# Performance work log

Measured on AMD Instinct MI355X. Metric: run time of the kernel, lower is better.

Reference implementation:

```python
import jax, jax.numpy as jnp
import numpy as np

ADIM = 128
VDIM = 64

def setup_inputs() -> dict:
    key = jax.random.key(0)
    ks = jax.random.split(key, 12)
    B, N, E = 4, 10000, 320000
    pos_0 = jax.random.normal(ks[0], (B, N, 3), dtype=jnp.float32)
    pos_1 = jax.random.normal(ks[1], (B, N, 3), dtype=jnp.float32)
    src = jax.random.randint(ks[2], (E,), 0, N, dtype=jnp.int64)
    dst = jax.random.randint(ks[3], (E,), 0, N, dtype=jnp.int64)
    # parameters (torch default inits approximated; randn for VecLinear as in source)
    Wv = jax.random.normal(ks[4], (VDIM, 6), dtype=jnp.float32)
    def lin(k, fan_in, fan_out):
        kw, kb = jax.random.split(k)
        bound = 1.0 / np.sqrt(fan_in)
        W = jax.random.uniform(kw, (fan_out, fan_in), minval=-bound, maxval=bound, dtype=jnp.float32)
        b = jax.random.uniform(kb, (fan_out,), minval=-bound, maxval=bound, dtype=jnp.float32)
        return W, b
    W1, b1 = lin(ks[5], 6, ADIM)
    W2, b2 = lin(ks[6], ADIM, ADIM)
    W3, b3 = lin(ks[7], ADIM, ADIM)
    return {"pos_0": pos_0, "pos_1": pos_1, "src": src, "dst": dst,
            "Wv": Wv, "W1": W1, "b1": b1, "W2": W2, "b2": b2, "W3": W3, "b3": b3}

def _leaky(x):
    return jnp.where(x >= 0, x, 0.2 * x)

def reference(pos_0, pos_1, src, dst, Wv, W1, b1, W2, b2, W3, b3):
    # gather endpoint positions: (B, E, 3)
    p0s = jnp.take(pos_0, src, axis=1)
    p0d = jnp.take(pos_0, dst, axis=1)
    p1s = jnp.take(pos_1, src, axis=1)
    p1d = jnp.take(pos_1, dst, axis=1)
    # 6 relative vectors: (B, E, 6, 3)
    vecs = jnp.stack([p0d - p0s, p1d - p1s, p1s - p0s, p1d - p0d, p1s - p0d, p1d - p0s], axis=2)
    norms = jnp.sqrt(jnp.sum(vecs * vecs, axis=-1))  # (B, E, 6)
    h = _leaky(jnp.einsum('bei,oi->beo', norms, W1) + b1)
    h = _leaky(jnp.einsum('bei,oi->beo', h, W2) + b2)
    a_out = jnp.einsum('bei,oi->beo', h, W3) + b3  # (B, E, ADIM)
    v_out = jnp.einsum('oi,beik->beok', Wv, vecs) / 3  # (B, E, VDIM, 3)
    return (a_out, v_out)
```

## Files before the change

kernel.cpp:

```cpp
#include <hip/hip_runtime.h>

#define NB 4
#define NN 10000
#define NE 320000
#define EPB 128
#define NBLK ((NB * NE) / EPB)

typedef unsigned int uint;
typedef unsigned short ushort;
typedef __attribute__((ext_vector_type(8))) short short8;
typedef __attribute__((ext_vector_type(4))) float f32x4;

#define WS_W1T 0
#define WS_W2T 8192
#define WS_W3T 40960
#define WS_WVT 73728

static __device__ __forceinline__ ushort f2bf(float f) {
    uint u = __float_as_uint(f);
    u += 0x7fffu + ((u >> 16) & 1u);
    return (ushort)(u >> 16);
}
static __device__ __forceinline__ uint pack2(float a, float b) {
    return (uint)f2bf(a) | ((uint)f2bf(b) << 16);
}
static __device__ __forceinline__ uint cvtpk(float a, float b) {
    uint r;
    asm("v_cvt_pk_bf16_f32 %0, %1, %2" : "=v"(r) : "v"(a), "v"(b));
    return r;
}
static __device__ __forceinline__ short8 u4s8(uint4 v) {
    union { uint4 u; short8 s; } x; x.u = v; return x.s;
}
static __device__ __forceinline__ f32x4 MF(uint4 a, uint4 b, f32x4 c) {
    return __builtin_amdgcn_mfma_f32_16x16x32_bf16(u4s8(a), u4s8(b), c, 0, 0, 0);
}

__global__ void prep_kernel(const float* __restrict__ W1, const float* __restrict__ W2,
                            const float* __restrict__ W3, const float* __restrict__ Wv,
                            unsigned char* __restrict__ ws) {
    int tid = blockIdx.x * blockDim.x + threadIdx.x;
    if (tid < 4096) {
        const float* W = (tid < 2048) ? W2 : W3;
        uint4* dst = (uint4*)(ws + ((tid < 2048) ? WS_W2T : WS_W3T));
        int f = tid & 2047;
        int lane = f & 63, kt = (f >> 6) & 3, mt = (f >> 8) & 7;
        int la = lane >> 4, lm = lane & 15;
        int n = mt * 16 + lm;
        uint w[4];
        #pragma unroll
        for (int jw = 0; jw < 4; ++jw) {
            int j0 = jw * 2, j1 = j0 + 1;
            int k0 = kt * 32 + (j0 >> 2) * 16 + la * 4 + (j0 & 3);
            int k1 = kt * 32 + (j1 >> 2) * 16 + la * 4 + (j1 & 3);
            w[jw] = pack2(W[n * 128 + k0], W[n * 128 + k1]);
        }
        dst[f] = make_uint4(w[0], w[1], w[2], w[3]);
    } else if (tid < 4608) {
        int f = tid - 4096;
        int lane = f & 63, mt = f >> 6;
        int la = lane >> 4, lm = lane & 15;
        int n = mt * 16 + lm;
        uint w[4];
        #pragma unroll
        for (int jw = 0; jw < 4; ++jw) {
            int j0 = jw * 2, j1 = j0 + 1;
            int k0 = (j0 >> 2) * 16 + la * 4 + (j0 & 3);
            int k1 = (j1 >> 2) * 16 + la * 4 + (j1 & 3);
            float f0 = (k0 < 6) ? W1[n * 6 + k0] : 0.f;
            float f1 = (k1 < 6) ? W1[n * 6 + k1] : 0.f;
            w[jw] = pack2(f0, f1);
        }
        ((uint4*)(ws + WS_W1T))[f] = make_uint4(w[0], w[1], w[2], w[3]);
    } else if (tid < 5376) {
        int f = tid - 4608;
        int lane = f & 63, mt = f >> 6;
        int la = lane >> 4, lm = lane & 15;
        int row = mt * 16 + lm;
        int o = row / 3, c = row - o * 3;
        uint w[4];
        #pragma unroll
        for (int jw = 0; jw < 4; ++jw) {
            float vv[2];
            #pragma unroll
            for (int dc = 0; dc < 2; ++dc) {
                int j = jw * 2 + dc;
                int k = (j >> 2) * 16 + la * 4 + (j & 3);
                int i = k / 3, cc = k - i * 3;
                vv[dc] = (k < 18 && cc == c) ? Wv[o * 6 + i] * (1.f / 3.f) : 0.f;
            }
            w[jw] = pack2(vv[0], vv[1]);
        }
        ((uint4*)(ws + WS_WVT))[f] = make_uint4(w[0], w[1], w[2], w[3]);
    }
}

__global__ __launch_bounds__(256, 3)
void edge_kernel(const float* __restrict__ pos0, const float* __restrict__ pos1,
                 const int* __restrict__ src, const int* __restrict__ dstI,
                 const float* __restrict__ b1, const float* __restrict__ b2,
                 const float* __restrict__ b3,
                 const unsigned char* __restrict__ ws, float* __restrict__ out) {
    __shared__ float s_pts[128][13];
    __shared__ float s_vecs[128][20];
    __shared__ float s_norms[6][128];

    const int tid = threadIdx.x;
    const int lane = tid & 63;
    const int w = tid >> 6;
    const int lm = lane & 15;
    const int la = lane >> 4;
    const int ew0 = w * 32;

    const int bid = blockIdx.x;
    const int b = bid / (NE / EPB);
    const int e0 = (bid % (NE / EPB)) * EPB;
    const size_t eg0 = (size_t)b * NE + e0;

    const uint4* W1T = (const uint4*)(ws + WS_W1T);
    const uint4* W2T = (const uint4*)(ws + WS_W2T);
    const uint4* W3T = (const uint4*)(ws + WS_W3T);
    const uint4* WVT = (const uint4*)(ws + WS_WVT);

    {
        const int el = ew0 + (lane & 31);
        const int side = lane >> 5;
        const int e = e0 + el;
        const int node = side ? dstI[e] : src[e];
        const size_t pb = ((size_t)b * NN + node) * 3;
        float a0 = pos0[pb], a1 = pos0[pb + 1], a2 = pos0[pb + 2];
        float c0 = pos1[pb], c1 = pos1[pb + 1], c2 = pos1[pb + 2];
        s_pts[el][side * 3 + 0] = a0;
        s_pts[el][side * 3 + 1] = a1;
        s_pts[el][side * 3 + 2] = a2;
        s_pts[el][6 + side * 3 + 0] = c0;
        s_pts[el][6 + side * 3 + 1] = c1;
        s_pts[el][6 + side * 3 + 2] = c2;
    }

    {
        const int el = ew0 + (lane & 31);
        const int grp = lane >> 5;
        float P[12];
        #pragma unroll
        for (int i = 0; i < 12; ++i) P[i] = s_pts[el][i];
        if (grp == 0) {
            const int va[4] = {1, 3, 2, 3}, vbx[4] = {0, 2, 0, 1};
            float v[4][3];
            #pragma unroll
            for (int i = 0; i < 4; ++i) {
                #pragma unroll
                for (int c = 0; c < 3; ++c) v[i][c] = P[va[i] * 3 + c] - P[vbx[i] * 3 + c];
                s_norms[i][el] = sqrtf(v[i][0]*v[i][0] + v[i][1]*v[i][1] + v[i][2]*v[i][2]);
            }
            float4 t0 = {v[0][0], v[0][1], v[0][2], v[1][0]};
            float4 t1 = {v[1][1], v[1][2], v[2][0], v[2][1]};
            float4 t2 = {v[2][2], v[3][0], v[3][1], v[3][2]};
            *(float4*)&s_vecs[el][0] = t0;
            *(float4*)&s_vecs[el][4] = t1;
            *(float4*)&s_vecs[el][8] = t2;
        } else {
            float v4[3], v5[3];
            #pragma unroll
            for (int c = 0; c < 3; ++c) {
                v4[c] = P[6 + c] - P[3 + c];
                v5[c] = P[9 + c] - P[0 + c];
            }
            s_norms[4][el] = sqrtf(v4[0]*v4[0] + v4[1]*v4[1] + v4[2]*v4[2]);
            s_norms[5][el] = sqrtf(v5[0]*v5[0] + v5[1]*v5[1] + v5[2]*v5[2]);
            float4 t = {v4[0], v4[1], v4[2], v5[0]};
            *(float4*)&s_vecs[el][12] = t;
            float2 t2 = {v5[1], v5[2]};
            *(float2*)&s_vecs[el][16] = t2;
        }
    }

    const f32x4 zero4 = {0.f, 0.f, 0.f, 0.f};

    {
        uint4 vbv[2];
        #pragma unroll
        for (int nt = 0; nt < 2; ++nt) {
            const int e = ew0 + nt * 16 + lm;
            float4 q = *(const float4*)&s_vecs[e][la * 4];
            uint c2 = 0;
            if (la == 0) c2 = cvtpk(s_vecs[e][16], s_vecs[e][17]);
            vbv[nt] = make_uint4(cvtpk(q.x, q.y), cvtpk(q.z, q.w), c2, 0u);
        }
        uint4 wv[12];
        #pragma unroll
        for (int mt = 0; mt < 12; ++mt) wv[mt] = WVT[mt * 64 + lane];
        float* vout = out + (size_t)NB * NE * 128;
        #pragma unroll
        for (int mt = 0; mt < 12; ++mt)
            #pragma unroll
            for (int nt = 0; nt < 2; ++nt) {
                f32x4 av = MF(wv[mt], vbv[nt], zero4);
                const size_t e = eg0 + ew0 + nt * 16 + lm;
                *(f32x4*)&vout[e * 192 + mt * 16 + la * 4] = av;
            }
    }

    f32x4 acc[8][2];
    {
        uint4 vb1[2];
        #pragma unroll
        for (int nt = 0; nt < 2; ++nt) {
            const int e = ew0 + nt * 16 + lm;
            uint c0 = 0, c1 = 0;
            if (la == 0) {
                c0 = cvtpk(s_norms[0][e], s_norms[1][e]);
                c1 = cvtpk(s_norms[2][e], s_norms[3][e]);
            } else if (la == 1) {
                c0 = cvtpk(s_norms[4][e], s_norms[5][e]);
            }
            vb1[nt] = make_uint4(c0, c1, 0u, 0u);
        }
        uint4 w1f[8];
        #pragma unroll
        for (int mt = 0; mt < 8; ++mt) w1f[mt] = W1T[mt * 64 + lane];
        #pragma unroll
        for (int mt = 0; mt < 8; ++mt)
            #pragma unroll
            for (int nt = 0; nt < 2; ++nt)
                acc[mt][nt] = MF(w1f[mt], vb1[nt], zero4);
    }
    uint4 vb[2][4];
    #pragma unroll
    for (int mt = 0; mt < 8; ++mt) {
        f32x4 bc = *(const f32x4*)&b1[mt * 16 + la * 4];
        #pragma unroll
        for (int nt = 0; nt < 2; ++nt)
            #pragma unroll
            for (int r = 0; r < 4; ++r) {
                float x = acc[mt][nt][r] + bc[r];
                acc[mt][nt][r] = fmaxf(x, 0.2f * x);
            }
    }
    #pragma unroll
    for (int nt = 0; nt < 2; ++nt)
        #pragma unroll
        for (int kt = 0; kt < 4; ++kt)
            vb[nt][kt] = make_uint4(
                cvtpk(acc[2*kt][nt][0], acc[2*kt][nt][1]),
                cvtpk(acc[2*kt][nt][2], acc[2*kt][nt][3]),
                cvtpk(acc[2*kt+1][nt][0], acc[2*kt+1][nt][1]),
                cvtpk(acc[2*kt+1][nt][2], acc[2*kt+1][nt][3]));

    #pragma unroll
    for (int mt = 0; mt < 8; ++mt)
        #pragma unroll
        for (int nt = 0; nt < 2; ++nt) acc[mt][nt] = zero4;
    #pragma unroll
    for (int kt = 0; kt < 4; ++kt) {
        uint4 wf[8];
        #pragma unroll
        for (int mt = 0; mt < 8; ++mt) wf[mt] = W2T[(mt * 4 + kt) * 64 + lane];
        #pragma unroll
        for (int mt = 0; mt < 8; ++mt)
            #pragma unroll
            for (int nt = 0; nt < 2; ++nt)
                acc[mt][nt] = MF(wf[mt], vb[nt][kt], acc[mt][nt]);
    }
    #pragma unroll
    for (int mt = 0; mt < 8; ++mt) {
        f32x4 bc = *(const f32x4*)&b2[mt * 16 + la * 4];
        #pragma unroll
        for (int nt = 0; nt < 2; ++nt)
            #pragma unroll
            for (int r = 0; r < 4; ++r) {
                float x = acc[mt][nt][r] + bc[r];
                acc[mt][nt][r] = fmaxf(x, 0.2f * x);
            }
    }
    #pragma unroll
    for (int nt = 0; nt < 2; ++nt)
        #pragma unroll
        for (int kt = 0; kt < 4; ++kt)
            vb[nt][kt] = make_uint4(
                cvtpk(acc[2*kt][nt][0], acc[2*kt][nt][1]),
                cvtpk(acc[2*kt][nt][2], acc[2*kt][nt][3]),
                cvtpk(acc[2*kt+1][nt][0], acc[2*kt+1][nt][1]),
                cvtpk(acc[2*kt+1][nt][2], acc[2*kt+1][nt][3]));

    #pragma unroll
    for (int mt = 0; mt < 8; ++mt)
        #pragma unroll
        for (int nt = 0; nt < 2; ++nt) acc[mt][nt] = zero4;
    #pragma unroll
    for (int kt = 0; kt < 4; ++kt) {
        uint4 wf[8];
        #pragma unroll
        for (int mt = 0; mt < 8; ++mt) wf[mt] = W3T[(mt * 4 + kt) * 64 + lane];
        #pragma unroll
        for (int mt = 0; mt < 8; ++mt)
            #pragma unroll
            for (int nt = 0; nt < 2; ++nt)
                acc[mt][nt] = MF(wf[mt], vb[nt][kt], acc[mt][nt]);
    }
    #pragma unroll
    for (int mt = 0; mt < 8; ++mt) {
        f32x4 bc = *(const f32x4*)&b3[mt * 16 + la * 4];
        #pragma unroll
        for (int nt = 0; nt < 2; ++nt) {
            f32x4 v = acc[mt][nt] + bc;
            const size_t e = eg0 + ew0 + nt * 16 + lm;
            *(f32x4*)&out[e * 128 + mt * 16 + la * 4] = v;
        }
    }
}

extern "C" void kernel_launch(void* const* d_in, const int* in_sizes, int n_in,
                              void* d_out, int out_size, void* d_ws, size_t ws_size,
                              hipStream_t stream) {
    const float* pos0 = (const float*)d_in[0];
    const float* pos1 = (const float*)d_in[1];
    const int* src = (const int*)d_in[2];
    const int* dstI = (const int*)d_in[3];
    const float* Wv = (const float*)d_in[4];
    const float* W1 = (const float*)d_in[5];
    const float* b1 = (const float*)d_in[6];
    const float* W2 = (const float*)d_in[7];
    const float* b2 = (const float*)d_in[8];
    const float* W3 = (const float*)d_in[9];
    const float* b3 = (const float*)d_in[10];
    unsigned char* ws = (unsigned char*)d_ws;
    float* out = (float*)d_out;

    prep_kernel<<<dim3(21), dim3(256), 0, stream>>>(W1, W2, W3, Wv, ws);
    edge_kernel<<<dim3(NBLK), dim3(256), 0, stream>>>(pos0, pos1, src, dstI, b1, b2, b3, ws, out);
}
```

Before: 435.8 us.

## Split edge blocks into separate vector-output and MLP blocks, stage W2 in LDS

Doubles the grid so that even blocks compute only the vector output (Wv projection) and odd blocks compute only the three-layer MLP. Both kinds still gather the endpoint positions. The MLP blocks stage W2 into a 32KB shared-memory buffer and read it from LDS instead of global memory. The intent is to shorten each block's critical path and spread the two output streams across more blocks, at the cost of duplicated gathers and larger LDS use, which may lower occupancy. A __syncthreads now follows the W2 staging, and the early return in the vector-output blocks comes before that barrier, so every thread in a block takes the same path.

```diff
diff --git a/kernel.cpp b/kernel.cpp
--- a/kernel.cpp
+++ b/kernel.cpp
@@ -4,7 +4,8 @@
 #define NN 10000
 #define NE 320000
 #define EPB 128
-#define NBLK ((NB * NE) / EPB)
+#define NPAIR (NE / EPB)
+#define NBLK (2 * NB * NPAIR)
 
 typedef unsigned int uint;
 typedef unsigned short ushort;
@@ -101,9 +102,8 @@
                  const float* __restrict__ b1, const float* __restrict__ b2,
                  const float* __restrict__ b3,
                  const unsigned char* __restrict__ ws, float* __restrict__ out) {
-    __shared__ float s_pts[128][13];
-    __shared__ float s_vecs[128][20];
-    __shared__ float s_norms[6][128];
+    __shared__ __align__(16) char smem[42496];
+    float (*s_pts)[13] = (float(*)[13])smem;
 
     const int tid = threadIdx.x;
     const int lane = tid & 63;
@@ -111,20 +111,19 @@
     const int lm = lane & 15;
     const int la = lane >> 4;
     const int ew0 = w * 32;
+    const int el = ew0 + (lane & 31);
+    const int side = lane >> 5;
 
     const int bid = blockIdx.x;
-    const int b = bid / (NE / EPB);
-    const int e0 = (bid % (NE / EPB)) * EPB;
+    const int kind = bid & 1;
+    const int idx = bid >> 1;
+    const int b = idx / NPAIR;
+    const int e0 = (idx % NPAIR) * EPB;
     const size_t eg0 = (size_t)b * NE + e0;
 
-    const uint4* W1T = (const uint4*)(ws + WS_W1T);
-    const uint4* W2T = (const uint4*)(ws + WS_W2T);
-    const uint4* W3T = (const uint4*)(ws + WS_W3T);
-    const uint4* WVT = (const uint4*)(ws + WS_WVT);
+    const f32x4 zero4 = {0.f, 0.f, 0.f, 0.f};
 
     {
-        const int el = ew0 + (lane & 31);
-        const int side = lane >> 5;
         const int e = e0 + el;
         const int node = side ? dstI[e] : src[e];
         const size_t pb = ((size_t)b * NN + node) * 3;
@@ -138,46 +137,38 @@
         s_pts[el][6 + side * 3 + 2] = c2;
     }
 
-    {
-        const int el = ew0 + (lane & 31);
-        const int grp = lane >> 5;
-        float P[12];
-        #pragma unroll
-        for (int i = 0; i < 12; ++i) P[i] = s_pts[el][i];
-        if (grp == 0) {
-            const int va[4] = {1, 3, 2, 3}, vbx[4] = {0, 2, 0, 1};
-            float v[4][3];
-            #pragma unroll
-            for (int i = 0; i < 4; ++i) {
+    if (kind == 0) {
+        float (*s_vecs)[20] = (float(*)[20])(smem + 6656);
+        {
+            float P[12];
+            #pragma unroll
+            for (int i = 0; i < 12; ++i) P[i] = s_pts[el][i];
+            if (side == 0) {
+                const int va[4] = {1, 3, 2, 3}, vbx[4] = {0, 2, 0, 1};
+                float v[4][3];
                 #pragma unroll
-                for (int c = 0; c < 3; ++c) v[i][c] = P[va[i] * 3 + c] - P[vbx[i] * 3 + c];
-                s_norms[i][el] = sqrtf(v[i][0]*v[i][0] + v[i][1]*v[i][1] + v[i][2]*v[i][2]);
-            }
-            float4 t0 = {v[0][0], v[0][1], v[0][2], v[1][0]};
-            float4 t1 = {v[1][1], v[1][2], v[2][0], v[2][1]};
-            float4 t2 = {v[2][2], v[3][0], v[3][1], v[3][2]};
-            *(float4*)&s_vecs[el][0] = t0;
-            *(float4*)&s_vecs[el][4] = t1;
-            *(float4*)&s_vecs[el][8] = t2;
-        } else {
-            float v4[3], v5[3];
-            #pragma unroll
-            for (int c = 0; c < 3; ++c) {
-                v4[c] = P[6 + c] - P[3 + c];
-                v5[c] = P[9 + c] - P[0 + c];
-            }
-            s_norms[4][el] = sqrtf(v4[0]*v4[0] + v4[1]*v4[1] + v4[2]*v4[2]);
-            s_norms[5][el] = sqrtf(v5[0]*v5[0] + v5[1]*v5[1] + v5[2]*v5[2]);
-            float4 t = {v4[0], v4[1], v4[2], v5[0]};
-            *(float4*)&s_vecs[el][12] = t;
-            float2 t2 = {v5[1], v5[2]};
-            *(float2*)&s_vecs[el][16] = t2;
-        }
-    }
-
-    const f32x4 zero4 = {0.f, 0.f, 0.f, 0.f};
-
-    {
+                for (int i = 0; i < 4; ++i)
+                    #pragma unroll
+                    for (int c = 0; c < 3; ++c) v[i][c] = P[va[i] * 3 + c] - P[vbx[i] * 3 + c];
+                float4 t0 = {v[0][0], v[0][1], v[0][2], v[1][0]};
+                float4 t1 = {v[1][1], v[1][2], v[2][0], v[2][1]};
+                float4 t2 = {v[2][2], v[3][0], v[3][1], v[3][2]};
+                *(float4*)&s_vecs[el][0] = t0;
+                *(float4*)&s_vecs[el][4] = t1;
+                *(float4*)&s_vecs[el][8] = t2;
+            } else {
+                float v4[3], v5[3];
+                #pragma unroll
+                for (int c = 0; c < 3; ++c) {
+                    v4[c] = P[6 + c] - P[3 + c];
+                    v5[c] = P[9 + c] - P[0 + c];
+                }
+                float4 t = {v4[0], v4[1], v4[2], v5[0]};
+                *(float4*)&s_vecs[el][12] = t;
+                float2 t2 = {v5[1], v5[2]};
+                *(float2*)&s_vecs[el][16] = t2;
+            }
+        }
         uint4 vbv[2];
         #pragma unroll
         for (int nt = 0; nt < 2; ++nt) {
@@ -187,6 +178,7 @@
             if (la == 0) c2 = cvtpk(s_vecs[e][16], s_vecs[e][17]);
             vbv[nt] = make_uint4(cvtpk(q.x, q.y), cvtpk(q.z, q.w), c2, 0u);
         }
+        const uint4* WVT = (const uint4*)(ws + WS_WVT);
         uint4 wv[12];
         #pragma unroll
         for (int mt = 0; mt < 12; ++mt) wv[mt] = WVT[mt * 64 + lane];
@@ -199,7 +191,42 @@
                 const size_t e = eg0 + ew0 + nt * 16 + lm;
                 *(f32x4*)&vout[e * 192 + mt * 16 + la * 4] = av;
             }
-    }
+        return;
+    }
+
+    float* s_normf = (float*)(smem + 6656);
+    uint4* s_W2 = (uint4*)(smem + 6656 + 3072);
+
+    const uint4* W2T = (const uint4*)(ws + WS_W2T);
+    {
+        uint4 stg[8];
+        #pragma unroll
+        for (int it = 0; it < 8; ++it) stg[it] = W2T[it * 256 + tid];
+        #pragma unroll
+        for (int it = 0; it < 8; ++it) s_W2[it * 256 + tid] = stg[it];
+    }
+
+    {
+        float P[12];
+        #pragma unroll
+        for (int i = 0; i < 12; ++i) P[i] = s_pts[el][i];
+        if (side == 0) {
+            const int va[4] = {1, 3, 2, 3}, vbx[4] = {0, 2, 0, 1};
+            #pragma unroll
+            for (int i = 0; i < 4; ++i) {
+                float x = P[va[i] * 3 + 0] - P[vbx[i] * 3 + 0];
+                float y = P[va[i] * 3 + 1] - P[vbx[i] * 3 + 1];
+                float z = P[va[i] * 3 + 2] - P[vbx[i] * 3 + 2];
+                s_normf[i * 128 + el] = sqrtf(x * x + y * y + z * z);
+            }
+        } else {
+            float x4 = P[6] - P[3], y4 = P[7] - P[4], z4 = P[8] - P[5];
+            float x5 = P[9] - P[0], y5 = P[10] - P[1], z5 = P[11] - P[2];
+            s_normf[4 * 128 + el] = sqrtf(x4 * x4 + y4 * y4 + z4 * z4);
+            s_normf[5 * 128 + el] = sqrtf(x5 * x5 + y5 * y5 + z5 * z5);
+        }
+    }
+    __syncthreads();
 
     f32x4 acc[8][2];
     {
@@ -209,13 +236,14 @@
             const int e = ew0 + nt * 16 + lm;
             uint c0 = 0, c1 = 0;
             if (la == 0) {
-                c0 = cvtpk(s_norms[0][e], s_norms[1][e]);
-                c1 = cvtpk(s_norms[2][e], s_norms[3][e]);
+                c0 = cvtpk(s_normf[0 * 128 + e], s_normf[1 * 128 + e]);
+                c1 = cvtpk(s_normf[2 * 128 + e], s_normf[3 * 128 + e]);
             } else if (la == 1) {
-                c0 = cvtpk(s_norms[4][e], s_norms[5][e]);
+                c0 = cvtpk(s_normf[4 * 128 + e], s_normf[5 * 128 + e]);
             }
             vb1[nt] = make_uint4(c0, c1, 0u, 0u);
         }
+        const uint4* W1T = (const uint4*)(ws + WS_W1T);
         uint4 w1f[8];
         #pragma unroll
         for (int mt = 0; mt < 8; ++mt) w1f[mt] = W1T[mt * 64 + lane];
@@ -255,7 +283,7 @@
     for (int kt = 0; kt < 4; ++kt) {
         uint4 wf[8];
         #pragma unroll
-        for (int mt = 0; mt < 8; ++mt) wf[mt] = W2T[(mt * 4 + kt) * 64 + lane];
+        for (int mt = 0; mt < 8; ++mt) wf[mt] = s_W2[(mt * 4 + kt) * 64 + lane];
         #pragma unroll
         for (int mt = 0; mt < 8; ++mt)
             #pragma unroll
@@ -283,6 +311,7 @@
                 cvtpk(acc[2*kt+1][nt][0], acc[2*kt+1][nt][1]),
                 cvtpk(acc[2*kt+1][nt][2], acc[2*kt+1][nt][3]));
 
+    const uint4* W3T = (const uint4*)(ws + WS_W3T);
     #pragma unroll
     for (int mt = 0; mt < 8; ++mt)
         #pragma unroll
```

New measurement: 390.9 us. 1.11x faster.

## Make edge kernel persistent with prefetched gathers and LDS-resident W2

Applied to the files above, without the earlier changes.

The edge kernel becomes persistent: a 512-block grid where each block loops over edge tiles. W2 is staged into shared memory once per block and W1 fragments stay in registers. The next tile's node indices and positions are gathered during the current tile's compute, with vector scratch double-buffered. This targets per-block launch overhead, repeated weight loads and exposed gather latency. The costs are lower occupancy (launch bounds 3 to 2), more shared memory, and no barriers around the shared s_pts/s_norm buffers, which relies on each thread reading only its own or its wave's entries.

```diff
diff --git a/kernel.cpp b/kernel.cpp
--- a/kernel.cpp
+++ b/kernel.cpp
@@ -4,7 +4,9 @@
 #define NN 10000
 #define NE 320000
 #define EPB 128
-#define NBLK ((NB * NE) / EPB)
+#define NPAIR (NE / EPB)
+#define NT (NB * NPAIR)
+#define NPB 512
 
 typedef unsigned int uint;
 typedef unsigned short ushort;
@@ -95,15 +97,16 @@
     }
 }
 
-__global__ __launch_bounds__(256, 3)
+__global__ __launch_bounds__(256, 2)
 void edge_kernel(const float* __restrict__ pos0, const float* __restrict__ pos1,
                  const int* __restrict__ src, const int* __restrict__ dstI,
                  const float* __restrict__ b1, const float* __restrict__ b2,
                  const float* __restrict__ b3,
                  const unsigned char* __restrict__ ws, float* __restrict__ out) {
+    __shared__ uint4 s_W2[2048];
     __shared__ float s_pts[128][13];
-    __shared__ float s_vecs[128][20];
-    __shared__ float s_norms[6][128];
+    __shared__ float s_norm[6 * 128];
+    __shared__ float s_vec[2][128][20];
 
     const int tid = threadIdx.x;
     const int lane = tid & 63;
@@ -111,201 +114,225 @@
     const int lm = lane & 15;
     const int la = lane >> 4;
     const int ew0 = w * 32;
-
-    const int bid = blockIdx.x;
-    const int b = bid / (NE / EPB);
-    const int e0 = (bid % (NE / EPB)) * EPB;
-    const size_t eg0 = (size_t)b * NE + e0;
+    const int el = ew0 + (lane & 31);
+    const int side = lane >> 5;
 
     const uint4* W1T = (const uint4*)(ws + WS_W1T);
     const uint4* W2T = (const uint4*)(ws + WS_W2T);
     const uint4* W3T = (const uint4*)(ws + WS_W3T);
     const uint4* WVT = (const uint4*)(ws + WS_WVT);
 
+    #pragma unroll
+    for (int it = 0; it < 8; ++it) s_W2[it * 256 + tid] = W2T[it * 256 + tid];
+
+    uint4 w1f[8];
+    #pragma unroll
+    for (int mt = 0; mt < 8; ++mt) w1f[mt] = W1T[mt * 64 + lane];
+
+    float* vout = out + (size_t)NB * NE * 128;
+    const f32x4 zero4 = {0.f, 0.f, 0.f, 0.f};
+
+    __syncthreads();
+
+    const int t0 = blockIdx.x;
     {
-        const int el = ew0 + (lane & 31);
-        const int side = lane >> 5;
-        const int e = e0 + el;
-        const int node = side ? dstI[e] : src[e];
-        const size_t pb = ((size_t)b * NN + node) * 3;
-        float a0 = pos0[pb], a1 = pos0[pb + 1], a2 = pos0[pb + 2];
-        float c0 = pos1[pb], c1 = pos1[pb + 1], c2 = pos1[pb + 2];
-        s_pts[el][side * 3 + 0] = a0;
-        s_pts[el][side * 3 + 1] = a1;
-        s_pts[el][side * 3 + 2] = a2;
-        s_pts[el][6 + side * 3 + 0] = c0;
-        s_pts[el][6 + side * 3 + 1] = c1;
-        s_pts[el][6 + side * 3 + 2] = c2;
+        const int b0 = t0 / NPAIR;
+        const int e0p = (t0 - b0 * NPAIR) * EPB;
+        const int node = side ? dstI[e0p + el] : src[e0p + el];
+        const size_t pb = ((size_t)b0 * NN + node) * 3;
+        s_pts[el][side * 3 + 0] = pos0[pb + 0];
+        s_pts[el][side * 3 + 1] = pos0[pb + 1];
+        s_pts[el][side * 3 + 2] = pos0[pb + 2];
+        s_pts[el][6 + side * 3 + 0] = pos1[pb + 0];
+        s_pts[el][6 + side * 3 + 1] = pos1[pb + 1];
+        s_pts[el][6 + side * 3 + 2] = pos1[pb + 2];
     }
 
-    {
-        const int el = ew0 + (lane & 31);
-        const int grp = lane >> 5;
-        float P[12];
-        #pragma unroll
-        for (int i = 0; i < 12; ++i) P[i] = s_pts[el][i];
-        if (grp == 0) {
-            const int va[4] = {1, 3, 2, 3}, vbx[4] = {0, 2, 0, 1};
-            float v[4][3];
-            #pragma unroll
-            for (int i = 0; i < 4; ++i) {
-                #pragma unroll
-                for (int c = 0; c < 3; ++c) v[i][c] = P[va[i] * 3 + c] - P[vbx[i] * 3 + c];
-                s_norms[i][el] = sqrtf(v[i][0]*v[i][0] + v[i][1]*v[i][1] + v[i][2]*v[i][2]);
-            }
-            float4 t0 = {v[0][0], v[0][1], v[0][2], v[1][0]};
-            float4 t1 = {v[1][1], v[1][2], v[2][0], v[2][1]};
-            float4 t2 = {v[2][2], v[3][0], v[3][1], v[3][2]};
-            *(float4*)&s_vecs[el][0] = t0;
-            *(float4*)&s_vecs[el][4] = t1;
-            *(float4*)&s_vecs[el][8] = t2;
-        } else {
-            float v4[3], v5[3];
-            #pragma unroll
-            for (int c = 0; c < 3; ++c) {
-                v4[c] = P[6 + c] - P[3 + c];
-                v5[c] = P[9 + c] - P[0 + c];
-            }
-            s_norms[4][el] = sqrtf(v4[0]*v4[0] + v4[1]*v4[1] + v4[2]*v4[2]);
-            s_norms[5][el] = sqrtf(v5[0]*v5[0] + v5[1]*v5[1] + v5[2]*v5[2]);
-            float4 t = {v4[0], v4[1], v4[2], v5[0]};
-            *(float4*)&s_vecs[el][12] = t;
-            float2 t2 = {v5[1], v5[2]};
-            *(float2*)&s_vecs[el][16] = t2;
-        }
-    }
-
-    const f32x4 zero4 = {0.f, 0.f, 0.f, 0.f};
-
-    {
-        uint4 vbv[2];
-        #pragma unroll
-        for (int nt = 0; nt < 2; ++nt) {
-            const int e = ew0 + nt * 16 + lm;
-            float4 q = *(const float4*)&s_vecs[e][la * 4];
-            uint c2 = 0;
-            if (la == 0) c2 = cvtpk(s_vecs[e][16], s_vecs[e][17]);
-            vbv[nt] = make_uint4(cvtpk(q.x, q.y), cvtpk(q.z, q.w), c2, 0u);
-        }
-        uint4 wv[12];
-        #pragma unroll
-        for (int mt = 0; mt < 12; ++mt) wv[mt] = WVT[mt * 64 + lane];
-        float* vout = out + (size_t)NB * NE * 128;
-        #pragma unroll
-        for (int mt = 0; mt < 12; ++mt)
+    int itc = 0;
+    for (int t = t0; t < NT; t += NPB, ++itc) {
+        const int b = t / NPAIR;
+        const int e0 = (t - b * NPAIR) * EPB;
+        const size_t eg0 = (size_t)b * NE + e0;
+        float (*sv)[20] = s_vec[itc & 1];
+
+        const int tn = t + NPB;
+        const int tv = (tn < NT) ? tn : t;
+        const int bn = tv / NPAIR;
+        const int e0n = (tv - bn * NPAIR) * EPB;
+        const int noden = side ? dstI[e0n + el] : src[e0n + el];
+
+        {
+            float P[12];
+            #pragma unroll
+            for (int i = 0; i < 12; ++i) P[i] = s_pts[el][i];
+            if (side == 0) {
+                const int va[4] = {1, 3, 2, 3}, vbx[4] = {0, 2, 0, 1};
+                float v[4][3];
+                #pragma unroll
+                for (int i = 0; i < 4; ++i) {
+                    #pragma unroll
+                    for (int c = 0; c < 3; ++c) v[i][c] = P[va[i] * 3 + c] - P[vbx[i] * 3 + c];
+                    s_norm[i * 128 + el] = sqrtf(v[i][0]*v[i][0] + v[i][1]*v[i][1] + v[i][2]*v[i][2]);
+                }
+                float4 t0v = {v[0][0], v[0][1], v[0][2], v[1][0]};
+                float4 t1v = {v[1][1], v[1][2], v[2][0], v[2][1]};
+                float4 t2v = {v[2][2], v[3][0], v[3][1], v[3][2]};
+                *(float4*)&sv[el][0] = t0v;
+                *(float4*)&sv[el][4] = t1v;
+                *(float4*)&sv[el][8] = t2v;
+            } else {
+                float v4[3], v5[3];
+                #pragma unroll
+                for (int c = 0; c < 3; ++c) {
+                    v4[c] = P[6 + c] - P[3 + c];
+                    v5[c] = P[9 + c] - P[0 + c];
+                }
+                s_norm[4 * 128 + el] = sqrtf(v4[0]*v4[0] + v4[1]*v4[1] + v4[2]*v4[2]);
+                s_norm[5 * 128 + el] = sqrtf(v5[0]*v5[0] + v5[1]*v5[1] + v5[2]*v5[2]);
+                float4 tv4 = {v4[0], v4[1], v4[2], v5[0]};
+                *(float4*)&sv[el][12] = tv4;
+                float2 tv2 = {v5[1], v5[2]};
+                *(float2*)&sv[el][16] = tv2;
+            }
+        }
+
+        {
+            uint4 vbv[2];
             #pragma unroll
             for (int nt = 0; nt < 2; ++nt) {
-                f32x4 av = MF(wv[mt], vbv[nt], zero4);
+                const int e = ew0 + nt * 16 + lm;
+                float4 q = *(const float4*)&sv[e][la * 4];
+                uint c2 = 0;
+                if (la == 0) c2 = cvtpk(sv[e][16], sv[e][17]);
+                vbv[nt] = make_uint4(cvtpk(q.x, q.y), cvtpk(q.z, q.w), c2, 0u);
+            }
+            #pragma unroll
+            for (int mt = 0; mt < 12; ++mt) {
+                uint4 wvm = WVT[mt * 64 + lane];
+                #pragma unroll
+                for (int nt = 0; nt < 2; ++nt) {
+                    f32x4 av = MF(wvm, vbv[nt], zero4);
+                    const size_t e = eg0 + ew0 + nt * 16 + lm;
+                    *(f32x4*)&vout[e * 192 + mt * 16 + la * 4] = av;
+                }
+            }
+        }
+
+        {
+            const size_t pbn = ((size_t)bn * NN + noden) * 3;
+            float a0 = pos0[pbn], a1 = pos0[pbn + 1], a2 = pos0[pbn + 2];
+            float c0 = pos1[pbn], c1 = pos1[pbn + 1], c2 = pos1[pbn + 2];
+            s_pts[el][side * 3 + 0] = a0;
+            s_pts[el][side * 3 + 1] = a1;
+            s_pts[el][side * 3 + 2] = a2;
+            s_pts[el][6 + side * 3 + 0] = c0;
+            s_pts[el][6 + side * 3 + 1] = c1;
+            s_pts[el][6 + side * 3 + 2] = c2;
+        }
+
+        f32x4 acc[8][2];
+        {
+            uint4 vb1[2];
+            #pragma unroll
+            for (int nt = 0; nt < 2; ++nt) {
+                const int e = ew0 + nt * 16 + lm;
+                uint c0 = 0, c1 = 0;
+                if (la == 0) {
+                    c0 = cvtpk(s_norm[0 * 128 + e], s_norm[1 * 128 + e]);
+                    c1 = cvtpk(s_norm[2 * 128 + e], s_norm[3 * 128 + e]);
+                } else if (la == 1) {
+                    c0 = cvtpk(s_norm[4 * 128 + e], s_norm[5 * 128 + e]);
+                }
+                vb1[nt] = make_uint4(c0, c1, 0u, 0u);
+            }
+            #pragma unroll
+            for (int mt = 0; mt < 8; ++mt)
+                #pragma unroll
+                for (int nt = 0; nt < 2; ++nt)
+                    acc[mt][nt] = MF(w1f[mt], vb1[nt], zero4);
+        }
+        uint4 vb[2][4];
+        #pragma unroll
+        for (int mt = 0; mt < 8; ++mt) {
+            f32x4 bc = *(const f32x4*)&b1[mt * 16 + la * 4];
+            #pragma unroll
+            for (int nt = 0; nt < 2; ++nt)
+                #pragma unroll
+                for (int r = 0; r < 4; ++r) {
+                    float x = acc[mt][nt][r] + bc[r];
+                    acc[mt][nt][r] = fmaxf(x, 0.2f * x);
+                }
+        }
+        #pragma unroll
+        for (int nt = 0; nt < 2; ++nt)
+            #pragma unroll
+            for (int kt = 0; kt < 4; ++kt)
+                vb[nt][kt] = make_uint4(
+                    cvtpk(acc[2*kt][nt][0], acc[2*kt][nt][1]),
+                    cvtpk(acc[2*kt][nt][2], acc[2*kt][nt][3]),
+                    cvtpk(acc[2*kt+1][nt][0], acc[2*kt+1][nt][1]),
+                    cvtpk(acc[2*kt+1][nt][2], acc[2*kt+1][nt][3]));
+
+        #pragma unroll
+        for (int mt = 0; mt < 8; ++mt)
+            #pragma unroll
+            for (int nt = 0; nt < 2; ++nt) acc[mt][nt] = zero4;
+        #pragma unroll
+        for (int kt = 0; kt < 4; ++kt) {
+            uint4 wf[8];
+            #pragma unroll
+            for (int mt = 0; mt < 8; ++mt) wf[mt] = s_W2[(mt * 4 + kt) * 64 + lane];
+            #pragma unroll
+            for (int mt = 0; mt < 8; ++mt)
+                #pragma unroll
+                for (int nt = 0; nt < 2; ++nt)
+                    acc[mt][nt] = MF(wf[mt], vb[nt][kt], acc[mt][nt]);
+        }
+        #pragma unroll
+        for (int mt = 0; mt < 8; ++mt) {
+            f32x4 bc = *(const f32x4*)&b2[mt * 16 + la * 4];
+            #pragma unroll
+            for (int nt = 0; nt < 2; ++nt)
+                #pragma unroll
+                for (int r = 0; r < 4; ++r) {
+                    float x = acc[mt][nt][r] + bc[r];
+                    acc[mt][nt][r] = fmaxf(x, 0.2f * x);
+                }
+        }
+        #pragma unroll
+        for (int nt = 0; nt < 2; ++nt)
+            #pragma unroll
+            for (int kt = 0; kt < 4; ++kt)
+                vb[nt][kt] = make_uint4(
+                    cvtpk(acc[2*kt][nt][0], acc[2*kt][nt][1]),
+                    cvtpk(acc[2*kt][nt][2], acc[2*kt][nt][3]),
+                    cvtpk(acc[2*kt+1][nt][0], acc[2*kt+1][nt][1]),
+                    cvtpk(acc[2*kt+1][nt][2], acc[2*kt+1][nt][3]));
+
+        #pragma unroll
+        for (int mt = 0; mt < 8; ++mt)
+            #pragma unroll
+            for (int nt = 0; nt < 2; ++nt) acc[mt][nt] = zero4;
+        #pragma unroll
+        for (int kt = 0; kt < 4; ++kt) {
+            uint4 wf[8];
+            #pragma unroll
+            for (int mt = 0; mt < 8; ++mt) wf[mt] = W3T[(mt * 4 + kt) * 64 + lane];
+            #pragma unroll
+            for (int mt = 0; mt < 8; ++mt)
+                #pragma unroll
+                for (int nt = 0; nt < 2; ++nt)
+                    acc[mt][nt] = MF(wf[mt], vb[nt][kt], acc[mt][nt]);
+        }
+        #pragma unroll
+        for (int mt = 0; mt < 8; ++mt) {
+            f32x4 bc = *(const f32x4*)&b3[mt * 16 + la * 4];
+            #pragma unroll
+            for (int nt = 0; nt < 2; ++nt) {
+                f32x4 v = acc[mt][nt] + bc;
                 const size_t e = eg0 + ew0 + nt * 16 + lm;
-                *(f32x4*)&vout[e * 192 + mt * 16 + la * 4] = av;
-            }
-    }
-
-    f32x4 acc[8][2];
-    {
-        uint4 vb1[2];
-        #pragma unroll
-        for (int nt = 0; nt < 2; ++nt) {
-            const int e = ew0 + nt * 16 + lm;
-            uint c0 = 0, c1 = 0;
-            if (la == 0) {
-                c0 = cvtpk(s_norms[0][e], s_norms[1][e]);
-                c1 = cvtpk(s_norms[2][e], s_norms[3][e]);
-            } else if (la == 1) {
-                c0 = cvtpk(s_norms[4][e], s_norms[5][e]);
-            }
-            vb1[nt] = make_uint4(c0, c1, 0u, 0u);
-        }
-        uint4 w1f[8];
-        #pragma unroll
-        for (int mt = 0; mt < 8; ++mt) w1f[mt] = W1T[mt * 64 + lane];
-        #pragma unroll
-        for (int mt = 0; mt < 8; ++mt)
-            #pragma unroll
-            for (int nt = 0; nt < 2; ++nt)
-                acc[mt][nt] = MF(w1f[mt], vb1[nt], zero4);
-    }
-    uint4 vb[2][4];
-    #pragma unroll
-    for (int mt = 0; mt < 8; ++mt) {
-        f32x4 bc = *(const f32x4*)&b1[mt * 16 + la * 4];
-        #pragma unroll
-        for (int nt = 0; nt < 2; ++nt)
-            #pragma unroll
-            for (int r = 0; r < 4; ++r) {
-                float x = acc[mt][nt][r] + bc[r];
-                acc[mt][nt][r] = fmaxf(x, 0.2f * x);
-            }
-    }
-    #pragma unroll
-    for (int nt = 0; nt < 2; ++nt)
-        #pragma unroll
-        for (int kt = 0; kt < 4; ++kt)
-            vb[nt][kt] = make_uint4(
-                cvtpk(acc[2*kt][nt][0], acc[2*kt][nt][1]),
-                cvtpk(acc[2*kt][nt][2], acc[2*kt][nt][3]),
-                cvtpk(acc[2*kt+1][nt][0], acc[2*kt+1][nt][1]),
-                cvtpk(acc[2*kt+1][nt][2], acc[2*kt+1][nt][3]));
-
-    #pragma unroll
-    for (int mt = 0; mt < 8; ++mt)
-        #pragma unroll
-        for (int nt = 0; nt < 2; ++nt) acc[mt][nt] = zero4;
-    #pragma unroll
-    for (int kt = 0; kt < 4; ++kt) {
-        uint4 wf[8];
-        #pragma unroll
-        for (int mt = 0; mt < 8; ++mt) wf[mt] = W2T[(mt * 4 + kt) * 64 + lane];
-        #pragma unroll
-        for (int mt = 0; mt < 8; ++mt)
-            #pragma unroll
-            for (int nt = 0; nt < 2; ++nt)
-                acc[mt][nt] = MF(wf[mt], vb[nt][kt], acc[mt][nt]);
-    }
-    #pragma unroll
-    for (int mt = 0; mt < 8; ++mt) {
-        f32x4 bc = *(const f32x4*)&b2[mt * 16 + la * 4];
-        #pragma unroll
-        for (int nt = 0; nt < 2; ++nt)
-            #pragma unroll
-            for (int r = 0; r < 4; ++r) {
-                float x = acc[mt][nt][r] + bc[r];
-                acc[mt][nt][r] = fmaxf(x, 0.2f * x);
-            }
-    }
-    #pragma unroll
-    for (int nt = 0; nt < 2; ++nt)
-        #pragma unroll
-        for (int kt = 0; kt < 4; ++kt)
-            vb[nt][kt] = make_uint4(
-                cvtpk(acc[2*kt][nt][0], acc[2*kt][nt][1]),
-                cvtpk(acc[2*kt][nt][2], acc[2*kt][nt][3]),
-                cvtpk(acc[2*kt+1][nt][0], acc[2*kt+1][nt][1]),
-                cvtpk(acc[2*kt+1][nt][2], acc[2*kt+1][nt][3]));
-
-    #pragma unroll
-    for (int mt = 0; mt < 8; ++mt)
-        #pragma unroll
-        for (int nt = 0; nt < 2; ++nt) acc[mt][nt] = zero4;
-    #pragma unroll
-    for (int kt = 0; kt < 4; ++kt) {
-        uint4 wf[8];
-        #pragma unroll
-        for (int mt = 0; mt < 8; ++mt) wf[mt] = W3T[(mt * 4 + kt) * 64 + lane];
-        #pragma unroll
-        for (int mt = 0; mt < 8; ++mt)
-            #pragma unroll
-            for (int nt = 0; nt < 2; ++nt)
-                acc[mt][nt] = MF(wf[mt], vb[nt][kt], acc[mt][nt]);
-    }
-    #pragma unroll
-    for (int mt = 0; mt < 8; ++mt) {
-        f32x4 bc = *(const f32x4*)&b3[mt * 16 + la * 4];
-        #pragma unroll
-        for (int nt = 0; nt < 2; ++nt) {
-            f32x4 v = acc[mt][nt] + bc;
-            const size_t e = eg0 + ew0 + nt * 16 + lm;
-            *(f32x4*)&out[e * 128 + mt * 16 + la * 4] = v;
+                *(f32x4*)&out[e * 128 + mt * 16 + la * 4] = v;
+            }
         }
     }
 }
@@ -328,5 +355,5 @@
     float* out = (float*)d_out;
 
     prep_kernel<<<dim3(21), dim3(256), 0, stream>>>(W1, W2, W3, Wv, ws);
-    edge_kernel<<<dim3(NBLK), dim3(256), 0, stream>>>(pos0, pos1, src, dstI, b1, b2, b3, ws, out);
-}
+    edge_kernel<<<dim3(NPB), dim3(256), 0, stream>>>(pos0, pos1, src, dstI, b1, b2, b3, ws, out);
+}
```

Result: slower. 610.7 us (+40.1%).
